# Kernel tuning notes

Measured on AMD Instinct MI355X. Metric: run time of the kernel, lower is better.

## Reference

```python
import jax, jax.numpy as jnp
import numpy as np

B, S, H, NH = 1, 2048, 2048, 32
HD = H // NH  # 64
DFF = 4 * H
EPS = 1e-5


def layer_norm(x, w, b):
    mu = jnp.mean(x, axis=-1, keepdims=True)
    var = jnp.var(x, axis=-1, keepdims=True)
    return (x - mu) * jax.lax.rsqrt(var + EPS) * w + b


def setup_inputs() -> dict:
    key = jax.random.key(0)
    ks = jax.random.split(key, 16)
    std = 0.02
    hidden_states = jax.random.normal(ks[0], (B, S, H), dtype=jnp.float32)
    # additive causal mask [1,1,S,S]
    causal = jnp.tril(jnp.ones((S, S), dtype=jnp.bool_))
    attention_mask = jnp.where(causal, 0.0, -1e9).astype(jnp.float32)[None, None]
    p = lambda k, shp: (jax.random.normal(k, shp, dtype=jnp.float32) * std)
    return {
        "hidden_states": hidden_states,
        "attention_mask": attention_mask,
        "ln1_w": jnp.ones((H,), jnp.float32), "ln1_b": jnp.zeros((H,), jnp.float32),
        "wq": p(ks[1], (H, H)), "bq": jnp.zeros((H,), jnp.float32),
        "wk": p(ks[2], (H, H)), "bk": jnp.zeros((H,), jnp.float32),
        "wv": p(ks[3], (H, H)), "bv": jnp.zeros((H,), jnp.float32),
        "wo": p(ks[4], (H, H)), "bo": jnp.zeros((H,), jnp.float32),
        "w1": p(ks[5], (H, DFF)), "b1": jnp.zeros((DFF,), jnp.float32),
        "w2": p(ks[6], (DFF, H)), "b2": jnp.zeros((H,), jnp.float32),
        "ln2_w": jnp.ones((H,), jnp.float32), "ln2_b": jnp.zeros((H,), jnp.float32),
    }


def reference(hidden_states, attention_mask, ln1_w, ln1_b, wq, bq, wk, bk, wv, bv,
              wo, bo, w1, b1, w2, b2, ln2_w, ln2_b):
    x = hidden_states
    # --- pre-norm attention ---
    residual = x
    h = layer_norm(x, ln1_w, ln1_b)
    scaling = HD ** -0.5
    q = (h @ wq + bq).reshape(B, S, NH, HD) * scaling
    k = (h @ wk + bk).reshape(B, S, NH, HD)
    v = (h @ wv + bv).reshape(B, S, NH, HD)
    scores = jnp.einsum('bqhd,bkhd->bhqk', q, k) + attention_mask
    p = jax.nn.softmax(scores, axis=-1)  # dropout is identity in eval
    attn = jnp.einsum('bhqk,bkhd->bqhd', p, v).reshape(B, S, H)
    attn = attn @ wo + bo
    x = residual + attn
    # --- pre-norm MLP ---
    residual = x
    h = layer_norm(x, ln2_w, ln2_b)
    h = jax.nn.gelu(h @ w1 + b1, approximate=False) @ w2 + b2
    return residual + h
```

## Files before the change

### kernel.cpp

```cpp
#include <hip/hip_runtime.h>
#include <math.h>

#define H 2048
#define S 2048
#define NH 32
#define HD 64
#define DFF 8192

typedef __attribute__((ext_vector_type(4))) float f32x4;
typedef __attribute__((ext_vector_type(8))) short short8;

static __device__ __forceinline__ ushort f2bf(float f) {
  unsigned u = __float_as_uint(f);
  u += 0x7fff + ((u >> 16) & 1);
  return (ushort)(u >> 16);
}

static __device__ __forceinline__ void gl_lds16(const ushort* g, ushort* l) {
  __builtin_amdgcn_global_load_lds(
      (__attribute__((address_space(1))) const void*)g,
      (__attribute__((address_space(3))) void*)l, 16, 0, 0);
}

__global__ __launch_bounds__(256) void transpose_cast_kernel(
    const float* __restrict__ W, ushort* __restrict__ Wt, int K, int N) {
  __shared__ __align__(16) ushort tile[64][72];
  int n0 = blockIdx.x * 64, k0 = blockIdx.y * 64;
  int t = threadIdx.x;
  int lk = t >> 4;
  int ln4 = (t & 15) * 4;
#pragma unroll
  for (int p = 0; p < 4; p++) {
    int k = p * 16 + lk;
    float4 v = *reinterpret_cast<const float4*>(&W[(size_t)(k0 + k) * N + n0 + ln4]);
    float vv[4] = {v.x, v.y, v.z, v.w};
#pragma unroll
    for (int i = 0; i < 4; i++) {
      int row = ln4 + i;
      int slot = ((k >> 3) ^ (row & 7));
      tile[row][(slot << 3) + (k & 7)] = f2bf(vv[i]);
    }
  }
  __syncthreads();
  int n = t >> 2;
  int kq = (t & 3) * 8;
#pragma unroll
  for (int p = 0; p < 2; p++) {
    int kk = kq + p * 32;
    int slot = ((kk >> 3) ^ (n & 7));
    short8 o = *reinterpret_cast<const short8*>(&tile[n][slot << 3]);
    *reinterpret_cast<short8*>(&Wt[(size_t)(n0 + n) * K + k0 + kk]) = o;
  }
}

__global__ __launch_bounds__(256) void vtrans_kernel(
    const ushort* __restrict__ V, ushort* __restrict__ VT) {
  __shared__ ushort tile[32][33];
  int s0 = blockIdx.x * 32, d0 = blockIdx.y * 32;
  int tx = threadIdx.x & 31, ty = threadIdx.x >> 5;
#pragma unroll
  for (int i = 0; i < 4; i++)
    tile[ty * 4 + i][tx] = V[(size_t)(s0 + ty * 4 + i) * H + d0 + tx];
  __syncthreads();
#pragma unroll
  for (int i = 0; i < 4; i++)
    VT[(size_t)(d0 + ty * 4 + i) * S + s0 + tx] = tile[tx][ty * 4 + i];
}

__global__ __launch_bounds__(256) void biascat_kernel(
    const float* __restrict__ bq, const float* __restrict__ bk,
    const float* __restrict__ bv, float* __restrict__ o) {
  int t = blockIdx.x * 256 + threadIdx.x;
  o[t] = (t < H) ? bq[t] : (t < 2 * H) ? bk[t - H] : bv[t - 2 * H];
}

__global__ __launch_bounds__(256) void ln_kernel(
    const float* __restrict__ x, const float* __restrict__ w,
    const float* __restrict__ b, ushort* __restrict__ out) {
  int row = blockIdx.x, t = threadIdx.x;
  const float4* xr = reinterpret_cast<const float4*>(x + (size_t)row * H);
  float4 v0 = xr[t * 2], v1 = xr[t * 2 + 1];
  float s = v0.x + v0.y + v0.z + v0.w + v1.x + v1.y + v1.z + v1.w;
  float q = v0.x * v0.x + v0.y * v0.y + v0.z * v0.z + v0.w * v0.w +
            v1.x * v1.x + v1.y * v1.y + v1.z * v1.z + v1.w * v1.w;
#pragma unroll
  for (int off = 32; off > 0; off >>= 1) {
    s += __shfl_down(s, off, 64);
    q += __shfl_down(q, off, 64);
  }
  __shared__ float sm[8];
  int lane = t & 63, wv = t >> 6;
  if (lane == 0) { sm[wv] = s; sm[wv + 4] = q; }
  __syncthreads();
  s = sm[0] + sm[1] + sm[2] + sm[3];
  q = sm[4] + sm[5] + sm[6] + sm[7];
  float mu = s * (1.0f / H);
  float var = q * (1.0f / H) - mu * mu;
  float rs = rsqrtf(var + 1e-5f);
  const float4* wr = reinterpret_cast<const float4*>(w);
  const float4* br = reinterpret_cast<const float4*>(b);
  float4 w0 = wr[t * 2], w1v = wr[t * 2 + 1], b0 = br[t * 2], b1v = br[t * 2 + 1];
  short8 pk;
  pk[0] = (short)f2bf((v0.x - mu) * rs * w0.x + b0.x);
  pk[1] = (short)f2bf((v0.y - mu) * rs * w0.y + b0.y);
  pk[2] = (short)f2bf((v0.z - mu) * rs * w0.z + b0.z);
  pk[3] = (short)f2bf((v0.w - mu) * rs * w0.w + b0.w);
  pk[4] = (short)f2bf((v1.x - mu) * rs * w1v.x + b1v.x);
  pk[5] = (short)f2bf((v1.y - mu) * rs * w1v.y + b1v.y);
  pk[6] = (short)f2bf((v1.z - mu) * rs * w1v.z + b1v.z);
  pk[7] = (short)f2bf((v1.w - mu) * rs * w1v.w + b1v.w);
  *reinterpret_cast<short8*>(out + (size_t)row * H + t * 8) = pk;
}

__global__ __launch_bounds__(256) void combine4_kernel(
    const float* __restrict__ res, const float* __restrict__ p0,
    const float* __restrict__ p1, const float* __restrict__ p2,
    const float* __restrict__ p3, const float* __restrict__ bias,
    float* __restrict__ out) {
  size_t i = (size_t)blockIdx.x * 256 + threadIdx.x;
  float4 a = reinterpret_cast<const float4*>(res)[i];
  float4 c0 = reinterpret_cast<const float4*>(p0)[i];
  float4 c1 = reinterpret_cast<const float4*>(p1)[i];
  float4 c2 = reinterpret_cast<const float4*>(p2)[i];
  float4 c3 = reinterpret_cast<const float4*>(p3)[i];
  int col = (int)((i * 4) & (H - 1));
  float4 bb = *reinterpret_cast<const float4*>(bias + col);
  float4 o;
  o.x = a.x + c0.x + c1.x + c2.x + c3.x + bb.x;
  o.y = a.y + c0.y + c1.y + c2.y + c3.y + bb.y;
  o.z = a.z + c0.z + c1.z + c2.z + c3.z + bb.z;
  o.w = a.w + c0.w + c1.w + c2.w + c3.w + bb.w;
  reinterpret_cast<float4*>(out)[i] = o;
}

__global__ __launch_bounds__(256) void combine_ln_kernel(
    const float* __restrict__ res, const float* __restrict__ p0,
    const float* __restrict__ p1, const float* __restrict__ bias,
    const float* __restrict__ lw, const float* __restrict__ lb,
    float* __restrict__ xout, ushort* __restrict__ lnout) {
  int row = blockIdx.x, t = threadIdx.x;
  const float4* rr = reinterpret_cast<const float4*>(res + (size_t)row * H);
  const float4* r0 = reinterpret_cast<const float4*>(p0 + (size_t)row * H);
  const float4* r1 = reinterpret_cast<const float4*>(p1 + (size_t)row * H);
  const float4* bb = reinterpret_cast<const float4*>(bias);
  float4 a0 = rr[t * 2], a1 = rr[t * 2 + 1];
  float4 c0 = r0[t * 2], c1 = r0[t * 2 + 1];
  float4 d0 = r1[t * 2], d1 = r1[t * 2 + 1];
  float4 e0 = bb[t * 2], e1 = bb[t * 2 + 1];
  float4 v0, v1;
  v0.x = a0.x + c0.x + d0.x + e0.x;
  v0.y = a0.y + c0.y + d0.y + e0.y;
  v0.z = a0.z + c0.z + d0.z + e0.z;
  v0.w = a0.w + c0.w + d0.w + e0.w;
  v1.x = a1.x + c1.x + d1.x + e1.x;
  v1.y = a1.y + c1.y + d1.y + e1.y;
  v1.z = a1.z + c1.z + d1.z + e1.z;
  v1.w = a1.w + c1.w + d1.w + e1.w;
  float4* xo = reinterpret_cast<float4*>(xout + (size_t)row * H);
  xo[t * 2] = v0;
  xo[t * 2 + 1] = v1;
  float s = v0.x + v0.y + v0.z + v0.w + v1.x + v1.y + v1.z + v1.w;
  float q = v0.x * v0.x + v0.y * v0.y + v0.z * v0.z + v0.w * v0.w +
            v1.x * v1.x + v1.y * v1.y + v1.z * v1.z + v1.w * v1.w;
#pragma unroll
  for (int off = 32; off > 0; off >>= 1) {
    s += __shfl_down(s, off, 64);
    q += __shfl_down(q, off, 64);
  }
  __shared__ float sm[8];
  int lane = t & 63, wv = t >> 6;
  if (lane == 0) { sm[wv] = s; sm[wv + 4] = q; }
  __syncthreads();
  s = sm[0] + sm[1] + sm[2] + sm[3];
  q = sm[4] + sm[5] + sm[6] + sm[7];
  float mu = s * (1.0f / H);
  float var = q * (1.0f / H) - mu * mu;
  float rs = rsqrtf(var + 1e-5f);
  const float4* wr = reinterpret_cast<const float4*>(lw);
  const float4* br = reinterpret_cast<const float4*>(lb);
  float4 w0 = wr[t * 2], w1v = wr[t * 2 + 1], b0 = br[t * 2], b1v = br[t * 2 + 1];
  short8 pk;
  pk[0] = (short)f2bf((v0.x - mu) * rs * w0.x + b0.x);
  pk[1] = (short)f2bf((v0.y - mu) * rs * w0.y + b0.y);
  pk[2] = (short)f2bf((v0.z - mu) * rs * w0.z + b0.z);
  pk[3] = (short)f2bf((v0.w - mu) * rs * w0.w + b0.w);
  pk[4] = (short)f2bf((v1.x - mu) * rs * w1v.x + b1v.x);
  pk[5] = (short)f2bf((v1.y - mu) * rs * w1v.y + b1v.y);
  pk[6] = (short)f2bf((v1.z - mu) * rs * w1v.z + b1v.z);
  pk[7] = (short)f2bf((v1.w - mu) * rs * w1v.w + b1v.w);
  *reinterpret_cast<short8*>(lnout + (size_t)row * H + t * 8) = pk;
}

template <int MODE>
__global__ __launch_bounds__(512, 2) void gemm256_kernel(
    const ushort* __restrict__ A, const ushort* __restrict__ Bt,
    const float* __restrict__ bias,
    ushort* __restrict__ outb, float* __restrict__ outf,
    int M, int N, int lda, int kbeg, int klen) {
  __shared__ __align__(16) ushort As[2][256 * 64];
  __shared__ __align__(16) ushort Bs[2][256 * 64];
  int tid = threadIdx.x, lane = tid & 63, w = tid >> 6;
  int lm = lane & 15, kg = lane >> 4;
  int wr = w >> 2, wc = w & 3;
  int gx = gridDim.x, nwg = gx * gridDim.y;
  int orig = blockIdx.y * gx + blockIdx.x;
  int wg = (orig & 7) * (nwg >> 3) + (orig >> 3);
  int m0 = (wg % gx) * 256, n0 = (wg / gx) * 256;
  int kb0 = kbeg + blockIdx.z * klen;

  f32x4 acc[8][4] = {};

  const ushort* srcA[4];
  const ushort* srcB[4];
  int dbase[4];
#pragma unroll
  for (int q = 0; q < 4; q++) {
    int g = q * 512 + tid;
    int row = g >> 3, gc = g & 7;
    int col = (gc ^ (row & 7)) << 3;
    srcA[q] = A + (size_t)(m0 + row) * lda + kb0 + col;
    srcB[q] = Bt + (size_t)(n0 + row) * lda + kb0 + col;
    dbase[q] = (q * 512 + w * 64) * 8;
  }

  const ushort* aB0 = &As[0][(wr * 128 + lm) * 64 + ((kg ^ (lm & 7)) << 3)];
  const ushort* aB1 = &As[0][(wr * 128 + lm) * 64 + (((4 + kg) ^ (lm & 7)) << 3)];
  const ushort* bB0 = &Bs[0][(wc * 64 + lm) * 64 + ((kg ^ (lm & 7)) << 3)];
  const ushort* bB1 = &Bs[0][(wc * 64 + lm) * 64 + (((4 + kg) ^ (lm & 7)) << 3)];

  int nK = klen >> 6;
  gl_lds16(srcB[0], &Bs[0][dbase[0]]);
  gl_lds16(srcB[1], &Bs[0][dbase[1]]);
  gl_lds16(srcB[2], &Bs[0][dbase[2]]);
  gl_lds16(srcB[3], &Bs[0][dbase[3]]);
  gl_lds16(srcA[0], &As[0][dbase[0]]);
  gl_lds16(srcA[2], &As[0][dbase[2]]);
  gl_lds16(srcA[1], &As[0][dbase[1]]);
  gl_lds16(srcA[3], &As[0][dbase[3]]);
  asm volatile("s_waitcnt vmcnt(2)" ::: "memory");
  __builtin_amdgcn_s_barrier();

  for (int kt = 0; kt < nK; kt++) {
    int cur = kt & 1, nxt = cur ^ 1;
    bool hn = (kt + 1 < nK);
    int ko = (kt + 1) << 6;
    const ushort* a0 = aB0 + cur * 16384;
    const ushort* a1 = aB1 + cur * 16384;
    const ushort* b0 = bB0 + cur * 16384;
    const ushort* b1 = bB1 + cur * 16384;

    short8 af[4][2], bf0[2][2], bf1[2][2];

#pragma unroll
    for (int i = 0; i < 4; i++) {
      af[i][0] = *reinterpret_cast<const short8*>(a0 + i * 1024);
      af[i][1] = *reinterpret_cast<const short8*>(a1 + i * 1024);
    }
#pragma unroll
    for (int n = 0; n < 2; n++) {
      bf0[n][0] = *reinterpret_cast<const short8*>(b0 + n * 1024);
      bf0[n][1] = *reinterpret_cast<const short8*>(b1 + n * 1024);
    }
    if (hn) {
      gl_lds16(srcB[0] + ko, &Bs[nxt][dbase[0]]);
      gl_lds16(srcB[1] + ko, &Bs[nxt][dbase[1]]);
    }
    __builtin_amdgcn_s_barrier();
    asm volatile("s_waitcnt lgkmcnt(0)" ::: "memory");
    __builtin_amdgcn_sched_barrier(0);
    __builtin_amdgcn_s_setprio(1);
#pragma unroll
    for (int i = 0; i < 4; i++)
#pragma unroll
      for (int n = 0; n < 2; n++)
#pragma unroll
        for (int s = 0; s < 2; s++)
          acc[i][n] = __builtin_amdgcn_mfma_f32_16x16x32_bf16(af[i][s], bf0[n][s], acc[i][n], 0, 0, 0);
    __builtin_amdgcn_s_setprio(0);
    __builtin_amdgcn_s_barrier();

#pragma unroll
    for (int n = 0; n < 2; n++) {
      bf1[n][0] = *reinterpret_cast<const short8*>(b0 + 2048 + n * 1024);
      bf1[n][1] = *reinterpret_cast<const short8*>(b1 + 2048 + n * 1024);
    }
    if (hn) {
      gl_lds16(srcB[2] + ko, &Bs[nxt][dbase[2]]);
      gl_lds16(srcB[3] + ko, &Bs[nxt][dbase[3]]);
    }
    __builtin_amdgcn_s_barrier();
    asm volatile("s_waitcnt lgkmcnt(0)" ::: "memory");
    __builtin_amdgcn_sched_barrier(0);
    __builtin_amdgcn_s_setprio(1);
#pragma unroll
    for (int i = 0; i < 4; i++)
#pragma unroll
      for (int n = 0; n < 2; n++)
#pragma unroll
        for (int s = 0; s < 2; s++)
          acc[i][2 + n] = __builtin_amdgcn_mfma_f32_16x16x32_bf16(af[i][s], bf1[n][s], acc[i][2 + n], 0, 0, 0);
    __builtin_amdgcn_s_setprio(0);
    if (hn) asm volatile("s_waitcnt vmcnt(4)" ::: "memory");
    else    asm volatile("s_waitcnt vmcnt(0)" ::: "memory");
    __builtin_amdgcn_s_barrier();

#pragma unroll
    for (int i = 0; i < 4; i++) {
      af[i][0] = *reinterpret_cast<const short8*>(a0 + 4096 + i * 1024);
      af[i][1] = *reinterpret_cast<const short8*>(a1 + 4096 + i * 1024);
    }
    if (hn) {
      gl_lds16(srcA[0] + ko, &As[nxt][dbase[0]]);
      gl_lds16(srcA[2] + ko, &As[nxt][dbase[2]]);
    }
    __builtin_amdgcn_s_barrier();
    asm volatile("s_waitcnt lgkmcnt(0)" ::: "memory");
    __builtin_amdgcn_sched_barrier(0);
    __builtin_amdgcn_s_setprio(1);
#pragma unroll
    for (int i = 0; i < 4; i++)
#pragma unroll
      for (int n = 0; n < 2; n++)
#pragma unroll
        for (int s = 0; s < 2; s++)
          acc[4 + i][n] = __builtin_amdgcn_mfma_f32_16x16x32_bf16(af[i][s], bf0[n][s], acc[4 + i][n], 0, 0, 0);
    __builtin_amdgcn_s_setprio(0);
    __builtin_amdgcn_s_barrier();

    if (hn) {
      gl_lds16(srcA[1] + ko, &As[nxt][dbase[1]]);
      gl_lds16(srcA[3] + ko, &As[nxt][dbase[3]]);
    }
    __builtin_amdgcn_s_barrier();
    __builtin_amdgcn_s_setprio(1);
#pragma unroll
    for (int i = 0; i < 4; i++)
#pragma unroll
      for (int n = 0; n < 2; n++)
#pragma unroll
        for (int s = 0; s < 2; s++)
          acc[4 + i][2 + n] = __builtin_amdgcn_mfma_f32_16x16x32_bf16(af[i][s], bf1[n][s], acc[4 + i][2 + n], 0, 0, 0);
    __builtin_amdgcn_s_setprio(0);
    if (hn) asm volatile("s_waitcnt vmcnt(2)" ::: "memory");
    __builtin_amdgcn_s_barrier();
  }

#pragma unroll
  for (int mi = 0; mi < 8; mi++) {
#pragma unroll
    for (int ni = 0; ni < 4; ni++) {
#pragma unroll
      for (int r = 0; r < 4; r++) {
        int row = m0 + wr * 128 + mi * 16 + kg * 4 + r;
        int col = n0 + wc * 64 + ni * 16 + lm;
        float v = acc[mi][ni][r];
        if (MODE == 0) {
          float t = v + bias[col];
          float sc = (col < H) ? 0.125f : 1.0f;
          size_t idx = (size_t)(col >> 11) * ((size_t)S * H) + (size_t)row * H + (col & (H - 1));
          outb[idx] = f2bf(t * sc);
        } else if (MODE == 1) {
          float t = v + bias[col];
          outb[(size_t)row * N + col] = f2bf(0.5f * t * (1.0f + erff(t * 0.70710678118f)));
        } else {
          int zs = blockIdx.z + ((blockIdx.z >> 1) << 1);
          outf[(size_t)zs * M * N + (size_t)row * N + col] = v;
        }
      }
    }
  }
}

__global__ __launch_bounds__(512) void attn_kernel(
    const ushort* __restrict__ Q, const ushort* __restrict__ Kmat,
    const ushort* __restrict__ VT, ushort* __restrict__ ctx) {
  __shared__ __align__(16) ushort Ks[2][128 * 64];
  __shared__ __align__(16) ushort Vs[2][64 * 128];
  __shared__ __align__(16) ushort Ps[8 * 16 * 64];
  int h = blockIdx.x;
  int x = blockIdx.y;
  int tid = threadIdx.x, lane = tid & 63, w = tid >> 6;
  int lm = lane & 15, kg = lane >> 4;

  int qbA = x, qbB = 15 - x;
  int tA = x + 1;
  const int nt = 17;

  short8 qa[2];
#pragma unroll
  for (int ks = 0; ks < 2; ks++)
    qa[ks] = *reinterpret_cast<const short8*>(
        Q + (size_t)(qbA * 128 + w * 16 + lm) * H + h * 64 + ks * 32 + kg * 8);

  float m_run[4], l_run[4];
  f32x4 o_acc[4] = {};
#pragma unroll
  for (int r = 0; r < 4; r++) { m_run[r] = -1e30f; l_run[r] = 0.f; }

  auto stage = [&](int kb, int buf) {
#pragma unroll
    for (int p = 0; p < 2; p++) {
      int gbase = p * 512 + w * 64;
      int gran = gbase + lane;
      int krow = gran >> 3, gk = gran & 7;
      gl_lds16(Kmat + (size_t)(kb * 128 + krow) * H + h * 64 + ((gk ^ (krow & 7)) << 3),
               &Ks[buf][gbase * 8]);
    }
#pragma unroll
    for (int p = 0; p < 2; p++) {
      int gbase = p * 512 + w * 64;
      int gran = gbase + lane;
      int vrow = gran >> 4, gv = gran & 15;
      gl_lds16(VT + (size_t)(h * 64 + vrow) * S + kb * 128 + ((gv ^ (vrow & 15)) << 3),
               &Vs[buf][gbase * 8]);
    }
  };

  stage(0, 0);
  __syncthreads();

  for (int t = 0; t < nt; t++) {
    int cur = t & 1;
    if (t + 1 < nt) {
      int tn = t + 1;
      stage((tn < tA) ? tn : tn - tA, cur ^ 1);
    }
    bool diag = (t == tA - 1) || (t == nt - 1);

    f32x4 sacc[8] = {};
#pragma unroll
    for (int j = 0; j < 8; j++) {
      int krow = j * 16 + lm;
#pragma unroll
      for (int ks = 0; ks < 2; ks++) {
        short8 kf = *reinterpret_cast<const short8*>(
            &Ks[cur][krow * 64 + (((ks * 4 + kg) ^ (lm & 7)) << 3)]);
        sacc[j] = __builtin_amdgcn_mfma_f32_16x16x32_bf16(qa[ks], kf, sacc[j], 0, 0, 0);
      }
    }
    if (diag) {
#pragma unroll
      for (int j = 0; j < 8; j++)
#pragma unroll
        for (int r = 0; r < 4; r++)
          if (j * 16 + lm > w * 16 + kg * 4 + r) sacc[j][r] = -1e30f;
    }

#pragma unroll
    for (int r = 0; r < 4; r++) {
      float mx = sacc[0][r];
#pragma unroll
      for (int j = 1; j < 8; j++) mx = fmaxf(mx, sacc[j][r]);
      mx = fmaxf(mx, __shfl_xor(mx, 1, 64));
      mx = fmaxf(mx, __shfl_xor(mx, 2, 64));
      mx = fmaxf(mx, __shfl_xor(mx, 4, 64));
      mx = fmaxf(mx, __shfl_xor(mx, 8, 64));
      float mnew = fmaxf(m_run[r], mx);
      float sc = __expf(m_run[r] - mnew);
      m_run[r] = mnew;
      float ps = 0.f;
#pragma unroll
      for (int j = 0; j < 8; j++) {
        float p = __expf(sacc[j][r] - mnew);
        sacc[j][r] = p;
        ps += p;
      }
      ps += __shfl_xor(ps, 1, 64);
      ps += __shfl_xor(ps, 2, 64);
      ps += __shfl_xor(ps, 4, 64);
      ps += __shfl_xor(ps, 8, 64);
      l_run[r] = l_run[r] * sc + ps;
#pragma unroll
      for (int jd = 0; jd < 4; jd++) o_acc[jd][r] *= sc;
    }

#pragma unroll
    for (int c = 0; c < 2; c++) {
#pragma unroll
      for (int jj = 0; jj < 4; jj++)
#pragma unroll
        for (int r = 0; r < 4; r++) {
          int rl = kg * 4 + r;
          int col = jj * 16 + lm;
          Ps[w * 1024 + rl * 64 + (((col >> 3) ^ (rl & 7)) << 3) + (col & 7)] =
              f2bf(sacc[c * 4 + jj][r]);
        }
      short8 pa[2];
#pragma unroll
      for (int ks = 0; ks < 2; ks++)
        pa[ks] = *reinterpret_cast<const short8*>(
            &Ps[w * 1024 + lm * 64 + (((ks * 4 + kg) ^ (lm & 7)) << 3)]);
#pragma unroll
      for (int jd = 0; jd < 4; jd++) {
        int d = jd * 16 + lm;
#pragma unroll
        for (int ks = 0; ks < 2; ks++) {
          short8 vf = *reinterpret_cast<const short8*>(
              &Vs[cur][d * 128 + (((c * 8 + ks * 4 + kg) ^ lm) << 3)]);
          o_acc[jd] = __builtin_amdgcn_mfma_f32_16x16x32_bf16(pa[ks], vf, o_acc[jd], 0, 0, 0);
        }
      }
    }

    if (t == tA - 1) {
#pragma unroll
      for (int jd = 0; jd < 4; jd++)
#pragma unroll
        for (int r = 0; r < 4; r++)
          ctx[(size_t)(qbA * 128 + w * 16 + kg * 4 + r) * H + h * 64 + jd * 16 + lm] =
              f2bf(o_acc[jd][r] / l_run[r]);
#pragma unroll
      for (int r = 0; r < 4; r++) { m_run[r] = -1e30f; l_run[r] = 0.f; }
#pragma unroll
      for (int jd = 0; jd < 4; jd++) o_acc[jd] = f32x4{0.f, 0.f, 0.f, 0.f};
#pragma unroll
      for (int ks = 0; ks < 2; ks++)
        qa[ks] = *reinterpret_cast<const short8*>(
            Q + (size_t)(qbB * 128 + w * 16 + lm) * H + h * 64 + ks * 32 + kg * 8);
    }
    __syncthreads();
  }

#pragma unroll
  for (int jd = 0; jd < 4; jd++)
#pragma unroll
    for (int r = 0; r < 4; r++)
      ctx[(size_t)(qbB * 128 + w * 16 + kg * 4 + r) * H + h * 64 + jd * 16 + lm] =
          f2bf(o_acc[jd][r] / l_run[r]);
}

extern "C" void kernel_launch(void* const* d_in, const int* in_sizes, int n_in,
                              void* d_out, int out_size, void* d_ws, size_t ws_size,
                              hipStream_t stream) {
  const float* x = (const float*)d_in[0];
  const float* ln1w = (const float*)d_in[2];
  const float* ln1b = (const float*)d_in[3];
  const float* wq = (const float*)d_in[4];
  const float* bq = (const float*)d_in[5];
  const float* wk = (const float*)d_in[6];
  const float* bk = (const float*)d_in[7];
  const float* wv = (const float*)d_in[8];
  const float* bv = (const float*)d_in[9];
  const float* wo = (const float*)d_in[10];
  const float* bo = (const float*)d_in[11];
  const float* w1 = (const float*)d_in[12];
  const float* b1 = (const float*)d_in[13];
  const float* w2 = (const float*)d_in[14];
  const float* b2 = (const float*)d_in[15];
  const float* ln2w = (const float*)d_in[16];
  const float* ln2b = (const float*)d_in[17];
  float* out = (float*)d_out;

  char* ws = (char*)d_ws;
  const size_t MB = 1024 * 1024;
  const size_t SH = (size_t)S * H;
  ushort* WT_QKV = (ushort*)(ws);
  ushort* WT_O = (ushort*)(ws + 24 * MB);
  ushort* WT_1 = (ushort*)(ws + 32 * MB);
  ushort* WT_2 = (ushort*)(ws + 64 * MB);
  ushort* LNO = (ushort*)(ws + 96 * MB);
  ushort* QKVB = (ushort*)(ws + 104 * MB);
  ushort* VTb = (ushort*)(ws + 128 * MB);
  ushort* CTX = (ushort*)(ws + 136 * MB);
  float* X1 = (float*)(ws + 144 * MB);
  float* BIASQ = (float*)(ws + 160 * MB);
  ushort* MID = (ushort*)(ws);
  float* SPA = (float*)(ws + 104 * MB);
  float* SPM = (float*)(ws + 32 * MB);

  transpose_cast_kernel<<<dim3(H / 64, H / 64), 256, 0, stream>>>(wq, WT_QKV, H, H);
  transpose_cast_kernel<<<dim3(H / 64, H / 64), 256, 0, stream>>>(wk, WT_QKV + SH, H, H);
  transpose_cast_kernel<<<dim3(H / 64, H / 64), 256, 0, stream>>>(wv, WT_QKV + 2 * SH, H, H);
  transpose_cast_kernel<<<dim3(H / 64, H / 64), 256, 0, stream>>>(wo, WT_O, H, H);
  transpose_cast_kernel<<<dim3(DFF / 64, H / 64), 256, 0, stream>>>(w1, WT_1, H, DFF);
  transpose_cast_kernel<<<dim3(H / 64, DFF / 64), 256, 0, stream>>>(w2, WT_2, DFF, H);
  biascat_kernel<<<3 * H / 256, 256, 0, stream>>>(bq, bk, bv, BIASQ);

  ln_kernel<<<S, 256, 0, stream>>>(x, ln1w, ln1b, LNO);

  gemm256_kernel<0><<<dim3(S / 256, 3 * H / 256), 512, 0, stream>>>(
      LNO, WT_QKV, BIASQ, QKVB, nullptr, S, 3 * H, H, 0, H);

  vtrans_kernel<<<dim3(S / 32, H / 32), 256, 0, stream>>>(QKVB + 2 * SH, VTb);

  attn_kernel<<<dim3(NH, 8), 512, 0, stream>>>(QKVB, QKVB + SH, VTb, CTX);

  gemm256_kernel<3><<<dim3(S / 256, H / 256, 2), 512, 0, stream>>>(
      CTX, WT_O, nullptr, nullptr, SPA, S, H, H, 0, H / 2);
  combine_ln_kernel<<<S, 256, 0, stream>>>(x, SPA, SPA + SH, bo, ln2w, ln2b, X1, LNO);

  gemm256_kernel<1><<<dim3(S / 256, DFF / 256), 512, 0, stream>>>(
      LNO, WT_1, b1, MID, nullptr, S, DFF, H, 0, H);

  gemm256_kernel<3><<<dim3(S / 256, H / 256, 4), 512, 0, stream>>>(
      MID, WT_2, nullptr, nullptr, SPM, S, H, DFF, 0, DFF / 4);
  combine4_kernel<<<SH / 1024, 256, 0, stream>>>(
      X1, SPM, SPM + SH, SPM + 4 * SH, SPM + 5 * SH, b2, out);
}
```

Measured before the change: 427.4 us.

## Parameterize GEMM N-tile width and merge four weight transposes into one launch

Templates the 256-row GEMM on the number of 16-wide N sub-tiles per wave, so the tile can be 192 or 128 columns. The QKV projection now uses 192-wide tiles and the out-projection uses 128-wide tiles, giving more workgroups to fill the CUs on these smaller grids. The four HxH weight transpose/cast launches are merged into a single launch over a z dimension to cut launch overhead. Narrower tiles lower arithmetic intensity per block, and the vmcnt wait counts had to be retuned per variant, which risks subtle pipeline hazards.

```diff
diff --git a/kernel.cpp b/kernel.cpp
--- a/kernel.cpp
+++ b/kernel.cpp
@@ -20,6 +20,43 @@
   __builtin_amdgcn_global_load_lds(
       (__attribute__((address_space(1))) const void*)g,
       (__attribute__((address_space(3))) void*)l, 16, 0, 0);
+}
+
+__global__ __launch_bounds__(256) void transpose4_kernel(
+    const float* __restrict__ w0, const float* __restrict__ w1,
+    const float* __restrict__ w2, const float* __restrict__ w3,
+    ushort* __restrict__ o0, ushort* __restrict__ o1,
+    ushort* __restrict__ o2, ushort* __restrict__ o3) {
+  __shared__ __align__(16) ushort tile[64][72];
+  int z = blockIdx.z;
+  const float* W = (z == 0) ? w0 : (z == 1) ? w1 : (z == 2) ? w2 : w3;
+  ushort* Wt = (z == 0) ? o0 : (z == 1) ? o1 : (z == 2) ? o2 : o3;
+  int n0 = blockIdx.x * 64, k0 = blockIdx.y * 64;
+  int t = threadIdx.x;
+  int lk = t >> 4;
+  int ln4 = (t & 15) * 4;
+#pragma unroll
+  for (int p = 0; p < 4; p++) {
+    int k = p * 16 + lk;
+    float4 v = *reinterpret_cast<const float4*>(&W[(size_t)(k0 + k) * H + n0 + ln4]);
+    float vv[4] = {v.x, v.y, v.z, v.w};
+#pragma unroll
+    for (int i = 0; i < 4; i++) {
+      int row = ln4 + i;
+      int slot = ((k >> 3) ^ (row & 7));
+      tile[row][(slot << 3) + (k & 7)] = f2bf(vv[i]);
+    }
+  }
+  __syncthreads();
+  int n = t >> 2;
+  int kq = (t & 3) * 8;
+#pragma unroll
+  for (int p = 0; p < 2; p++) {
+    int kk = kq + p * 32;
+    int slot = ((kk >> 3) ^ (n & 7));
+    short8 o = *reinterpret_cast<const short8*>(&tile[n][slot << 3]);
+    *reinterpret_cast<short8*>(&Wt[(size_t)(n0 + n) * H + k0 + kk]) = o;
+  }
 }
 
 __global__ __launch_bounds__(256) void transpose_cast_kernel(
@@ -191,27 +228,31 @@
   *reinterpret_cast<short8*>(lnout + (size_t)row * H + t * 8) = pk;
 }
 
-template <int MODE>
+template <int MODE, int NI>
 __global__ __launch_bounds__(512, 2) void gemm256_kernel(
     const ushort* __restrict__ A, const ushort* __restrict__ Bt,
     const float* __restrict__ bias,
     ushort* __restrict__ outb, float* __restrict__ outf,
     int M, int N, int lda, int kbeg, int klen) {
+  constexpr int BN = NI * 64;
+  constexpr int NH0 = (NI + 1) / 2;
+  constexpr int NH1 = NI - NH0;
+  constexpr int BQ0 = (NI + 1) / 2;
   __shared__ __align__(16) ushort As[2][256 * 64];
-  __shared__ __align__(16) ushort Bs[2][256 * 64];
+  __shared__ __align__(16) ushort Bs[2][BN * 64];
   int tid = threadIdx.x, lane = tid & 63, w = tid >> 6;
   int lm = lane & 15, kg = lane >> 4;
   int wr = w >> 2, wc = w & 3;
   int gx = gridDim.x, nwg = gx * gridDim.y;
   int orig = blockIdx.y * gx + blockIdx.x;
   int wg = (orig & 7) * (nwg >> 3) + (orig >> 3);
-  int m0 = (wg % gx) * 256, n0 = (wg / gx) * 256;
+  int m0 = (wg % gx) * 256, n0 = (wg / gx) * BN;
   int kb0 = kbeg + blockIdx.z * klen;
 
-  f32x4 acc[8][4] = {};
+  f32x4 acc[8][NI] = {};
 
   const ushort* srcA[4];
-  const ushort* srcB[4];
+  const ushort* srcB[NI];
   int dbase[4];
 #pragma unroll
   for (int q = 0; q < 4; q++) {
@@ -219,20 +260,18 @@
     int row = g >> 3, gc = g & 7;
     int col = (gc ^ (row & 7)) << 3;
     srcA[q] = A + (size_t)(m0 + row) * lda + kb0 + col;
-    srcB[q] = Bt + (size_t)(n0 + row) * lda + kb0 + col;
+    if (q < NI) srcB[q] = Bt + (size_t)(n0 + row) * lda + kb0 + col;
     dbase[q] = (q * 512 + w * 64) * 8;
   }
 
   const ushort* aB0 = &As[0][(wr * 128 + lm) * 64 + ((kg ^ (lm & 7)) << 3)];
   const ushort* aB1 = &As[0][(wr * 128 + lm) * 64 + (((4 + kg) ^ (lm & 7)) << 3)];
-  const ushort* bB0 = &Bs[0][(wc * 64 + lm) * 64 + ((kg ^ (lm & 7)) << 3)];
-  const ushort* bB1 = &Bs[0][(wc * 64 + lm) * 64 + (((4 + kg) ^ (lm & 7)) << 3)];
+  const ushort* bB0 = &Bs[0][(wc * 16 * NI + lm) * 64 + ((kg ^ (lm & 7)) << 3)];
+  const ushort* bB1 = &Bs[0][(wc * 16 * NI + lm) * 64 + (((4 + kg) ^ (lm & 7)) << 3)];
 
   int nK = klen >> 6;
-  gl_lds16(srcB[0], &Bs[0][dbase[0]]);
-  gl_lds16(srcB[1], &Bs[0][dbase[1]]);
-  gl_lds16(srcB[2], &Bs[0][dbase[2]]);
-  gl_lds16(srcB[3], &Bs[0][dbase[3]]);
+#pragma unroll
+  for (int q = 0; q < NI; q++) gl_lds16(srcB[q], &Bs[0][dbase[q]]);
   gl_lds16(srcA[0], &As[0][dbase[0]]);
   gl_lds16(srcA[2], &As[0][dbase[2]]);
   gl_lds16(srcA[1], &As[0][dbase[1]]);
@@ -246,10 +285,10 @@
     int ko = (kt + 1) << 6;
     const ushort* a0 = aB0 + cur * 16384;
     const ushort* a1 = aB1 + cur * 16384;
-    const ushort* b0 = bB0 + cur * 16384;
-    const ushort* b1 = bB1 + cur * 16384;
-
-    short8 af[4][2], bf0[2][2], bf1[2][2];
+    const ushort* b0 = bB0 + cur * (BN * 64);
+    const ushort* b1 = bB1 + cur * (BN * 64);
+
+    short8 af[4][2], bf0[NH0][2], bf1[NH0][2];
 
 #pragma unroll
     for (int i = 0; i < 4; i++) {
@@ -257,13 +296,13 @@
       af[i][1] = *reinterpret_cast<const short8*>(a1 + i * 1024);
     }
 #pragma unroll
-    for (int n = 0; n < 2; n++) {
+    for (int n = 0; n < NH0; n++) {
       bf0[n][0] = *reinterpret_cast<const short8*>(b0 + n * 1024);
       bf0[n][1] = *reinterpret_cast<const short8*>(b1 + n * 1024);
     }
     if (hn) {
-      gl_lds16(srcB[0] + ko, &Bs[nxt][dbase[0]]);
-      gl_lds16(srcB[1] + ko, &Bs[nxt][dbase[1]]);
+#pragma unroll
+      for (int q = 0; q < BQ0; q++) gl_lds16(srcB[q] + ko, &Bs[nxt][dbase[q]]);
     }
     __builtin_amdgcn_s_barrier();
     asm volatile("s_waitcnt lgkmcnt(0)" ::: "memory");
@@ -272,7 +311,7 @@
 #pragma unroll
     for (int i = 0; i < 4; i++)
 #pragma unroll
-      for (int n = 0; n < 2; n++)
+      for (int n = 0; n < NH0; n++)
 #pragma unroll
         for (int s = 0; s < 2; s++)
           acc[i][n] = __builtin_amdgcn_mfma_f32_16x16x32_bf16(af[i][s], bf0[n][s], acc[i][n], 0, 0, 0);
@@ -280,13 +319,13 @@
     __builtin_amdgcn_s_barrier();
 
 #pragma unroll
-    for (int n = 0; n < 2; n++) {
-      bf1[n][0] = *reinterpret_cast<const short8*>(b0 + 2048 + n * 1024);
-      bf1[n][1] = *reinterpret_cast<const short8*>(b1 + 2048 + n * 1024);
+    for (int n = 0; n < NH1; n++) {
+      bf1[n][0] = *reinterpret_cast<const short8*>(b0 + (NH0 + n) * 1024);
+      bf1[n][1] = *reinterpret_cast<const short8*>(b1 + (NH0 + n) * 1024);
     }
     if (hn) {
-      gl_lds16(srcB[2] + ko, &Bs[nxt][dbase[2]]);
-      gl_lds16(srcB[3] + ko, &Bs[nxt][dbase[3]]);
+#pragma unroll
+      for (int q = BQ0; q < NI; q++) gl_lds16(srcB[q] + ko, &Bs[nxt][dbase[q]]);
     }
     __builtin_amdgcn_s_barrier();
     asm volatile("s_waitcnt lgkmcnt(0)" ::: "memory");
@@ -295,13 +334,18 @@
 #pragma unroll
     for (int i = 0; i < 4; i++)
 #pragma unroll
-      for (int n = 0; n < 2; n++)
+      for (int n = 0; n < NH1; n++)
 #pragma unroll
         for (int s = 0; s < 2; s++)
-          acc[i][2 + n] = __builtin_amdgcn_mfma_f32_16x16x32_bf16(af[i][s], bf1[n][s], acc[i][2 + n], 0, 0, 0);
+          acc[i][NH0 + n] = __builtin_amdgcn_mfma_f32_16x16x32_bf16(af[i][s], bf1[n][s], acc[i][NH0 + n], 0, 0, 0);
     __builtin_amdgcn_s_setprio(0);
-    if (hn) asm volatile("s_waitcnt vmcnt(4)" ::: "memory");
-    else    asm volatile("s_waitcnt vmcnt(0)" ::: "memory");
+    if (hn) {
+      if constexpr (NI == 4) asm volatile("s_waitcnt vmcnt(4)" ::: "memory");
+      else if constexpr (NI == 3) asm volatile("s_waitcnt vmcnt(3)" ::: "memory");
+      else asm volatile("s_waitcnt vmcnt(2)" ::: "memory");
+    } else {
+      asm volatile("s_waitcnt vmcnt(0)" ::: "memory");
+    }
     __builtin_amdgcn_s_barrier();
 
 #pragma unroll
@@ -320,7 +364,7 @@
 #pragma unroll
     for (int i = 0; i < 4; i++)
 #pragma unroll
-      for (int n = 0; n < 2; n++)
+      for (int n = 0; n < NH0; n++)
 #pragma unroll
         for (int s = 0; s < 2; s++)
           acc[4 + i][n] = __builtin_amdgcn_mfma_f32_16x16x32_bf16(af[i][s], bf0[n][s], acc[4 + i][n], 0, 0, 0);
@@ -336,10 +380,10 @@
 #pragma unroll
     for (int i = 0; i < 4; i++)
 #pragma unroll
-      for (int n = 0; n < 2; n++)
+      for (int n = 0; n < NH1; n++)
 #pragma unroll
         for (int s = 0; s < 2; s++)
-          acc[4 + i][2 + n] = __builtin_amdgcn_mfma_f32_16x16x32_bf16(af[i][s], bf1[n][s], acc[4 + i][2 + n], 0, 0, 0);
+          acc[4 + i][NH0 + n] = __builtin_amdgcn_mfma_f32_16x16x32_bf16(af[i][s], bf1[n][s], acc[4 + i][NH0 + n], 0, 0, 0);
     __builtin_amdgcn_s_setprio(0);
     if (hn) asm volatile("s_waitcnt vmcnt(2)" ::: "memory");
     __builtin_amdgcn_s_barrier();
@@ -348,11 +392,11 @@
 #pragma unroll
   for (int mi = 0; mi < 8; mi++) {
 #pragma unroll
-    for (int ni = 0; ni < 4; ni++) {
+    for (int ni = 0; ni < NI; ni++) {
 #pragma unroll
       for (int r = 0; r < 4; r++) {
         int row = m0 + wr * 128 + mi * 16 + kg * 4 + r;
-        int col = n0 + wc * 64 + ni * 16 + lm;
+        int col = n0 + wc * 16 * NI + ni * 16 + lm;
         float v = acc[mi][ni][r];
         if (MODE == 0) {
           float t = v + bias[col];
@@ -568,31 +612,29 @@
   float* SPA = (float*)(ws + 104 * MB);
   float* SPM = (float*)(ws + 32 * MB);
 
-  transpose_cast_kernel<<<dim3(H / 64, H / 64), 256, 0, stream>>>(wq, WT_QKV, H, H);
-  transpose_cast_kernel<<<dim3(H / 64, H / 64), 256, 0, stream>>>(wk, WT_QKV + SH, H, H);
-  transpose_cast_kernel<<<dim3(H / 64, H / 64), 256, 0, stream>>>(wv, WT_QKV + 2 * SH, H, H);
-  transpose_cast_kernel<<<dim3(H / 64, H / 64), 256, 0, stream>>>(wo, WT_O, H, H);
+  transpose4_kernel<<<dim3(H / 64, H / 64, 4), 256, 0, stream>>>(
+      wq, wk, wv, wo, WT_QKV, WT_QKV + SH, WT_QKV + 2 * SH, WT_O);
   transpose_cast_kernel<<<dim3(DFF / 64, H / 64), 256, 0, stream>>>(w1, WT_1, H, DFF);
   transpose_cast_kernel<<<dim3(H / 64, DFF / 64), 256, 0, stream>>>(w2, WT_2, DFF, H);
   biascat_kernel<<<3 * H / 256, 256, 0, stream>>>(bq, bk, bv, BIASQ);
 
   ln_kernel<<<S, 256, 0, stream>>>(x, ln1w, ln1b, LNO);
 
-  gemm256_kernel<0><<<dim3(S / 256, 3 * H / 256), 512, 0, stream>>>(
+  gemm256_kernel<0, 3><<<dim3(S / 256, 3 * H / 192), 512, 0, stream>>>(
       LNO, WT_QKV, BIASQ, QKVB, nullptr, S, 3 * H, H, 0, H);
 
   vtrans_kernel<<<dim3(S / 32, H / 32), 256, 0, stream>>>(QKVB + 2 * SH, VTb);
 
   attn_kernel<<<dim3(NH, 8), 512, 0, stream>>>(QKVB, QKVB + SH, VTb, CTX);
 
-  gemm256_kernel<3><<<dim3(S / 256, H / 256, 2), 512, 0, stream>>>(
+  gemm256_kernel<3, 2><<<dim3(S / 256, H / 128, 2), 512, 0, stream>>>(
       CTX, WT_O, nullptr, nullptr, SPA, S, H, H, 0, H / 2);
   combine_ln_kernel<<<S, 256, 0, stream>>>(x, SPA, SPA + SH, bo, ln2w, ln2b, X1, LNO);
 
-  gemm256_kernel<1><<<dim3(S / 256, DFF / 256), 512, 0, stream>>>(
+  gemm256_kernel<1, 4><<<dim3(S / 256, DFF / 256), 512, 0, stream>>>(
       LNO, WT_1, b1, MID, nullptr, S, DFF, H, 0, H);
 
-  gemm256_kernel<3><<<dim3(S / 256, H / 256, 4), 512, 0, stream>>>(
+  gemm256_kernel<3, 4><<<dim3(S / 256, H / 256, 4), 512, 0, stream>>>(
       MID, WT_2, nullptr, nullptr, SPM, S, H, DFF, 0, DFF / 4);
   combine4_kernel<<<SH / 1024, 256, 0, stream>>>(
       X1, SPM, SPM + SH, SPM + 4 * SH, SPM + 5 * SH, b2, out);
```

New measurement: 401.3 us. -6.1%, faster.
